# Kernel optimization log

Measured on AMD Instinct MI355X. Metric: run time of the kernel, lower is better.

The kernel has to match this reference:

```python
import jax, jax.numpy as jnp
import numpy as np

EMBED_DIM = 1024
NUM_HEADS = 16
HEAD_DIM = EMBED_DIM // NUM_HEADS
B, S = 4, 2048


def setup_inputs() -> dict:
    key = jax.random.key(0)
    ks = jax.random.split(key, 11)
    scale = 1.0 / np.sqrt(EMBED_DIM)
    def lin(k):
        kw, kb = jax.random.split(k)
        W = jax.random.uniform(kw, (EMBED_DIM, EMBED_DIM), jnp.float32, -scale, scale)
        b = jax.random.uniform(kb, (EMBED_DIM,), jnp.float32, -scale, scale)
        return W, b
    Wq, bq = lin(ks[0]); Wk, bk = lin(ks[1]); Wv, bv = lin(ks[2]); Wo, bo = lin(ks[3])
    return {
        "query": jax.random.normal(ks[4], (B, S, EMBED_DIM), jnp.float32),
        "key": jax.random.normal(ks[5], (B, S, EMBED_DIM), jnp.float32),
        "value": jax.random.normal(ks[6], (B, S, EMBED_DIM), jnp.float32),
        "Wq": Wq, "bq": bq, "Wk": Wk, "bk": bk, "Wv": Wv, "bv": bv, "Wo": Wo, "bo": bo,
    }


def reference(query, key, value, Wq, bq, Wk, bk, Wv, bv, Wo, bo):
    Bz, Sz, E = query.shape
    H, Dh = NUM_HEADS, HEAD_DIM
    # projections -> [B, H, S, Dh]
    q = (query @ Wq + bq).reshape(Bz, Sz, H, Dh).transpose(0, 2, 1, 3)
    k = (key @ Wk + bk).reshape(Bz, Sz, H, Dh).transpose(0, 2, 1, 3)
    v = (value @ Wv + bv).reshape(Bz, Sz, H, Dh).transpose(0, 2, 1, 3)
    scores = jnp.einsum('bhsd,bhtd->bhst', q, k) / jnp.sqrt(jnp.asarray(Dh, q.dtype))
    attn = jax.nn.softmax(scores, axis=-1)  # dropout is identity in eval mode
    out = jnp.einsum('bhst,bhtd->bhsd', attn, v)  # [B,H,S,Dh]
    out = out.transpose(0, 2, 1, 3).reshape(Bz, Sz, E)
    out = out @ Wo + bo
    return out, attn
```

## Files before the change

kernel.cpp:

```cpp
#include <hip/hip_runtime.h>
#include <stdint.h>


using bf16x8 = __attribute__((ext_vector_type(8))) short;
using f32x4  = __attribute__((ext_vector_type(4))) float;
using u16x4  = __attribute__((ext_vector_type(4))) unsigned short;
using u64x2  = __attribute__((ext_vector_type(2))) unsigned long long;

#define MFMA_BF16 __builtin_amdgcn_mfma_f32_16x16x32_bf16

__device__ __forceinline__ unsigned short f2bf(float x) {
    unsigned int u = __builtin_bit_cast(unsigned int, x);
    u = (u + 0x7FFFu + ((u >> 16) & 1u)) >> 16;
    return (unsigned short)u;
}
__device__ __forceinline__ float bf2f(unsigned short u) {
    return __builtin_bit_cast(float, (unsigned int)u << 16);
}
__device__ __forceinline__ float exp2_fast(float x) {
    float r; asm("v_exp_f32 %0, %1" : "=v"(r) : "v"(x)); return r;
}
__device__ __forceinline__ float log2_fast(float x) {
    float r; asm("v_log_f32 %0, %1" : "=v"(r) : "v"(x)); return r;
}
__device__ __forceinline__ void gload_lds16(const unsigned short* g, bf16x8* l) {
    __builtin_amdgcn_global_load_lds(
        (const __attribute__((address_space(1))) unsigned int*)(g),
        (__attribute__((address_space(3))) unsigned int*)(l), 16, 0, 0);
}

__global__ __launch_bounds__(256) void cvt_kernel(
    const float* __restrict__ q, const float* __restrict__ k,
    const float* __restrict__ v, unsigned short* __restrict__ dst)
{
    const float* src = (blockIdx.y == 0) ? q : (blockIdx.y == 1) ? k : v;
    unsigned short* d = dst + (size_t)blockIdx.y * 8388608;
    size_t i = ((size_t)blockIdx.x * 256 + threadIdx.x) * 8;
    float4 a = *(const float4*)(src + i);
    float4 b = *(const float4*)(src + i + 4);
    u16x4 lo = {f2bf(a.x), f2bf(a.y), f2bf(a.z), f2bf(a.w)};
    u16x4 hi = {f2bf(b.x), f2bf(b.y), f2bf(b.z), f2bf(b.w)};
    *(u16x4*)(d + i) = lo;
    *(u16x4*)(d + i + 4) = hi;
}

__global__ __launch_bounds__(256) void wtrans_kernel(
    const float* __restrict__ w0, const float* __restrict__ w1,
    const float* __restrict__ w2, const float* __restrict__ w3,
    unsigned short* __restrict__ Wt)
{
    __shared__ float tile[64][65];
    const float* src = (blockIdx.z == 0) ? w0 : (blockIdx.z == 1) ? w1 :
                       (blockIdx.z == 2) ? w2 : w3;
    unsigned short* dst = Wt + (size_t)blockIdx.z * (1u << 20);
    const int k0 = blockIdx.x * 64, n0 = blockIdx.y * 64;
    const int tid = threadIdx.x;
#pragma unroll
    for (int i = 0; i < 16; ++i) {
        int idx = i * 256 + tid;
        int kk = idx >> 6, nn = idx & 63;
        tile[kk][nn] = src[(size_t)(k0 + kk) * 1024 + n0 + nn];
    }
    __syncthreads();
#pragma unroll
    for (int i = 0; i < 16; ++i) {
        int idx = i * 256 + tid;
        int nn = idx >> 6, kk = idx & 63;
        dst[(size_t)(n0 + nn) * 1024 + k0 + kk] = f2bf(tile[kk][nn]);
    }
}

template<int OUT_MODE>
__global__ __launch_bounds__(256) void gemm_kernel(
    const unsigned short* __restrict__ A, const unsigned short* __restrict__ Bt,
    const float* __restrict__ bias, void* __restrict__ Cp, float prescale)
{
    __shared__ bf16x8 Alds[1024];
    __shared__ bf16x8 Blds[1024];
    const int tid = threadIdx.x;
    const int lane = tid & 63;
    const int w = tid >> 6;
    const int wm = w >> 1, wn = w & 1;
    const int m0 = blockIdx.x * 128, n0 = blockIdx.y * 128;
    const int r16 = lane & 15, g = lane >> 4;

    f32x4 acc[4][4] = {};

    for (int kt = 0; kt < 16; ++kt) {
        const int k0 = kt * 64;
#pragma unroll
        for (int issue = 0; issue < 4; ++issue) {
            int s = issue * 256 + tid;
            int row = s >> 3, cc = (s & 7) ^ (row & 7);
            gload_lds16(A  + (size_t)(m0 + row) * 1024 + k0 + cc * 8,
                        &Alds[issue * 256 + w * 64]);
            gload_lds16(Bt + (size_t)(n0 + row) * 1024 + k0 + cc * 8,
                        &Blds[issue * 256 + w * 64]);
        }
        __syncthreads();
#pragma unroll
        for (int ks = 0; ks < 2; ++ks) {
            bf16x8 af[4], bfr[4];
#pragma unroll
            for (int mf = 0; mf < 4; ++mf) {
                int row = wm * 64 + mf * 16 + r16;
                af[mf] = Alds[row * 8 + ((ks * 4 + g) ^ (row & 7))];
            }
#pragma unroll
            for (int nf = 0; nf < 4; ++nf) {
                int row = wn * 64 + nf * 16 + r16;
                bfr[nf] = Blds[row * 8 + ((ks * 4 + g) ^ (row & 7))];
            }
#pragma unroll
            for (int mf = 0; mf < 4; ++mf)
#pragma unroll
                for (int nf = 0; nf < 4; ++nf)
                    acc[mf][nf] = MFMA_BF16(af[mf], bfr[nf], acc[mf][nf], 0, 0, 0);
        }
        __syncthreads();
    }

#pragma unroll
    for (int nf = 0; nf < 4; ++nf) {
        const int n = n0 + wn * 64 + nf * 16 + r16;
        const float bv = bias[n];
#pragma unroll
        for (int mf = 0; mf < 4; ++mf) {
            const int mb = m0 + wm * 64 + mf * 16 + g * 4;
            if constexpr (OUT_MODE == 2) {
                float* C = (float*)Cp;
#pragma unroll
                for (int r = 0; r < 4; ++r)
                    C[(size_t)(mb + r) * 1024 + n] = acc[mf][nf][r] + bv;
            } else if constexpr (OUT_MODE == 0) {
                unsigned short* C = (unsigned short*)Cp;
                const int h = n >> 6, d = n & 63;
#pragma unroll
                for (int r = 0; r < 4; ++r) {
                    int m = mb + r;
                    int b = m >> 11, s2 = m & 2047;
                    C[((((size_t)b * 16 + h) * 2048 + s2) << 6) + d] =
                        f2bf((acc[mf][nf][r] + bv) * prescale);
                }
            } else {
                unsigned short* C = (unsigned short*)Cp;
                const int h = n >> 6, d = n & 63;
                const int b = mb >> 11, s2 = mb & 2047;
                u16x4 pk;
#pragma unroll
                for (int r = 0; r < 4; ++r) pk[r] = f2bf(acc[mf][nf][r] + bv);
                *(u16x4*)(C + (((size_t)b * 16 + h) * 64 + d) * 2048 + s2) = pk;
            }
        }
    }
}

__global__ __launch_bounds__(256) void attn_kernel(
    const unsigned short* __restrict__ Q,
    const unsigned short* __restrict__ K,
    const unsigned short* __restrict__ VT,
    float* __restrict__ attn,
    unsigned short* __restrict__ ctx)
{
    __shared__ bf16x8 k_buf[2][64 * 8];
    __shared__ bf16x8 v_buf[2][64 * 8];
    __shared__ unsigned long long p_buf[64 * 16];

    const int tid = threadIdx.x;
    const int lane = tid & 63;
    const int w = tid >> 6;
    const int L = blockIdx.x;
    const int xcd = L & 7, j = L >> 3;
    const int qt = j & 31;
    const int bh = ((j >> 5) << 3) | xcd;
    const int r16 = lane & 15, g = lane >> 4;

    const unsigned short* Kb = K + (size_t)bh * 2048 * 64;
    const unsigned short* Vb = VT + (size_t)bh * 64 * 2048;

    const int row0 = tid >> 3, cc0 = tid & 7;
    const int row1 = row0 + 32;
    const int kslot0 = row0 * 8 + (cc0 ^ (row0 & 7));
    const int kslot1 = row1 * 8 + (cc0 ^ (row1 & 7));

    const int qrow = w * 16 + r16;
    const unsigned short* qptr = Q + ((size_t)bh * 2048 + (size_t)qt * 64 + qrow) * 64 + g * 8;
    const bf16x8 qf0 = *(const bf16x8*)(qptr);
    const bf16x8 qf1 = *(const bf16x8*)(qptr + 32);

    k_buf[0][kslot0] = *(const bf16x8*)(Kb + (size_t)row0 * 64 + cc0 * 8);
    k_buf[0][kslot1] = *(const bf16x8*)(Kb + (size_t)row1 * 64 + cc0 * 8);
    bf16x8 pf0 = *(const bf16x8*)(Kb + 4096 + (size_t)row0 * 64 + cc0 * 8);
    bf16x8 pf1 = *(const bf16x8*)(Kb + 4096 + (size_t)row1 * 64 + cc0 * 8);
    __syncthreads();

    float l4[4] = {0.f, 0.f, 0.f, 0.f};
#pragma unroll 2
    for (int kt = 0; kt < 32; ++kt) {
        const int cur = kt & 1;
        bf16x8 nn0, nn1;
        if (kt + 2 < 32) {
            const unsigned short* src = Kb + (size_t)(kt + 2) * 4096;
            nn0 = *(const bf16x8*)(src + (size_t)row0 * 64 + cc0 * 8);
            nn1 = *(const bf16x8*)(src + (size_t)row1 * 64 + cc0 * 8);
        }
#pragma unroll
        for (int kf = 0; kf < 4; ++kf) {
            const int row = kf * 16 + r16;
            f32x4 t = {};
            t = MFMA_BF16(k_buf[cur][row * 8 + ((0 + g) ^ (row & 7))], qf0, t, 0, 0, 0);
            t = MFMA_BF16(k_buf[cur][row * 8 + ((4 + g) ^ (row & 7))], qf1, t, 0, 0, 0);
#pragma unroll
            for (int r = 0; r < 4; ++r) l4[r] += exp2_fast(t[r]);
        }
        if (kt + 1 < 32) {
            k_buf[cur ^ 1][kslot0] = pf0;
            k_buf[cur ^ 1][kslot1] = pf1;
        }
        __syncthreads();
        pf0 = nn0;
        pf1 = nn1;
    }
    float l_acc = (l4[0] + l4[1]) + (l4[2] + l4[3]);
    l_acc += __shfl_xor(l_acc, 16, 64);
    l_acc += __shfl_xor(l_acc, 32, 64);
    const float lg2invl = -log2_fast(l_acc);

    {
        bf16x8 a0 = *(const bf16x8*)(Kb + (size_t)row0 * 64 + cc0 * 8);
        bf16x8 a1 = *(const bf16x8*)(Kb + (size_t)row1 * 64 + cc0 * 8);
        bf16x8 b0 = *(const bf16x8*)(Vb + (size_t)row0 * 2048 + cc0 * 8);
        bf16x8 b1 = *(const bf16x8*)(Vb + (size_t)row1 * 2048 + cc0 * 8);
        k_buf[0][kslot0] = a0; k_buf[0][kslot1] = a1;
        v_buf[0][kslot0] = b0; v_buf[0][kslot1] = b1;
    }
    __syncthreads();

    float* attn_tile = attn + ((size_t)bh * 2048 + (size_t)qt * 64) * 2048;
    const f32x4 cinit = {lg2invl, lg2invl, lg2invl, lg2invl};

    f32x4 oacc[4] = {};
    for (int kt = 0; kt < 32; ++kt) {
        const int cur = kt & 1;
        bf16x8 nk0, nk1, nv0, nv1;
        if (kt != 31) {
            const unsigned short* ksrc = Kb + (size_t)(kt + 1) * 64 * 64;
            const unsigned short* vsrc = Vb + (size_t)(kt + 1) * 64;
            nk0 = *(const bf16x8*)(ksrc + (size_t)row0 * 64 + cc0 * 8);
            nk1 = *(const bf16x8*)(ksrc + (size_t)row1 * 64 + cc0 * 8);
            nv0 = *(const bf16x8*)(vsrc + (size_t)row0 * 2048 + cc0 * 8);
            nv1 = *(const bf16x8*)(vsrc + (size_t)row1 * 2048 + cc0 * 8);
        }
#pragma unroll
        for (int kf = 0; kf < 4; ++kf) {
            const int row = kf * 16 + r16;
            f32x4 t = cinit;
            t = MFMA_BF16(k_buf[cur][row * 8 + ((0 + g) ^ (row & 7))], qf0, t, 0, 0, 0);
            t = MFMA_BF16(k_buf[cur][row * 8 + ((4 + g) ^ (row & 7))], qf1, t, 0, 0, 0);
            u16x4 pk;
#pragma unroll
            for (int r = 0; r < 4; ++r) pk[r] = f2bf(exp2_fast(t[r]));
            const int c = 2 * kf + (g >> 1);
            p_buf[qrow * 16 + ((c ^ (qrow & 7)) << 1) + (g & 1)] =
                __builtin_bit_cast(unsigned long long, pk);
        }
#pragma unroll
        for (int i = 0; i < 2; ++i)
#pragma unroll
            for (int jj = 0; jj < 2; ++jj) {
                const int srow = w * 16 + i * 8 + (lane >> 3);
                const int col0 = jj * 32 + (lane & 7) * 4;
                const int c = col0 >> 3, half = (col0 >> 2) & 1;
                unsigned long long praw =
                    p_buf[srow * 16 + ((c ^ (srow & 7)) << 1) + half];
                u16x4 pk = __builtin_bit_cast(u16x4, praw);
                f32x4 pv = {bf2f(pk[0]), bf2f(pk[1]), bf2f(pk[2]), bf2f(pk[3])};
                __builtin_nontemporal_store(
                    pv, (f32x4*)(attn_tile + (size_t)srow * 2048 + kt * 64 + col0));
            }
#pragma unroll
        for (int ks = 0; ks < 2; ++ks) {
            const int cs = (ks * 4 + g) ^ (qrow & 7);
            u64x2 praw2 = {p_buf[qrow * 16 + cs * 2], p_buf[qrow * 16 + cs * 2 + 1]};
            bf16x8 a = __builtin_bit_cast(bf16x8, praw2);
#pragma unroll
            for (int df = 0; df < 4; ++df) {
                const int rowv = df * 16 + r16;
                oacc[df] = MFMA_BF16(a, v_buf[cur][rowv * 8 + ((ks * 4 + g) ^ (rowv & 7))],
                                     oacc[df], 0, 0, 0);
            }
        }
        if (kt != 31) {
            k_buf[cur ^ 1][kslot0] = nk0; k_buf[cur ^ 1][kslot1] = nk1;
            v_buf[cur ^ 1][kslot0] = nv0; v_buf[cur ^ 1][kslot1] = nv1;
        }
        __syncthreads();
    }

    const int b = bh >> 4, h = bh & 15;
#pragma unroll
    for (int df = 0; df < 4; ++df) {
        int d = df * 16 + r16;
#pragma unroll
        for (int r = 0; r < 4; ++r) {
            int s2 = qt * 64 + w * 16 + g * 4 + r;
            ctx[((size_t)b * 2048 + s2) * 1024 + h * 64 + d] = f2bf(oacc[df][r]);
        }
    }
}

extern "C" void kernel_launch(void* const* d_in, const int* in_sizes, int n_in,
                              void* d_out, int out_size, void* d_ws, size_t ws_size,
                              hipStream_t stream)
{
    (void)in_sizes; (void)n_in; (void)out_size; (void)ws_size;
    const float* query = (const float*)d_in[0];
    const float* key_  = (const float*)d_in[1];
    const float* value = (const float*)d_in[2];
    const float* Wq = (const float*)d_in[3];
    const float* bq = (const float*)d_in[4];
    const float* Wk = (const float*)d_in[5];
    const float* bk = (const float*)d_in[6];
    const float* Wv = (const float*)d_in[7];
    const float* bv = (const float*)d_in[8];
    const float* Wo = (const float*)d_in[9];
    const float* bo = (const float*)d_in[10];

    char* ws = (char*)d_ws;
    unsigned short* Wt  = (unsigned short*)(ws);
    unsigned short* qb  = (unsigned short*)(ws + ((size_t)8  << 20));
    unsigned short* kb  = (unsigned short*)(ws + ((size_t)24 << 20));
    unsigned short* vtb = (unsigned short*)(ws + ((size_t)40 << 20));
    unsigned short* ctx = (unsigned short*)(ws + ((size_t)56 << 20));
    float* outp = (float*)d_out;
    float* attn = outp + (size_t)4 * 2048 * 1024;

    const size_t ATTN_ELEMS = (size_t)64 * 2048 * 2048;
    const size_t STASH_FLOATS = (size_t)3 * 8388608 / 2;
    unsigned short* qkvb = (unsigned short*)(attn + (ATTN_ELEMS - STASH_FLOATS));
    unsigned short* qbf = qkvb;
    unsigned short* kbf = qkvb + 8388608;
    unsigned short* vbf = qkvb + 16777216;

    const float qscale = 0.125f * 1.44269504089f;

    cvt_kernel<<<dim3(4096, 3), 256, 0, stream>>>(query, key_, value, qkvb);
    wtrans_kernel<<<dim3(16, 16, 4), 256, 0, stream>>>(Wq, Wk, Wv, Wo, Wt);
    gemm_kernel<0><<<dim3(64, 8), 256, 0, stream>>>(qbf, Wt,              bq, qb,  qscale);
    gemm_kernel<0><<<dim3(64, 8), 256, 0, stream>>>(kbf, Wt + (1u << 20), bk, kb,  1.0f);
    gemm_kernel<1><<<dim3(64, 8), 256, 0, stream>>>(vbf, Wt + (2u << 20), bv, vtb, 1.0f);
    attn_kernel<<<dim3(2048), 256, 0, stream>>>(qb, kb, vtb, attn, ctx);
    gemm_kernel<2><<<dim3(64, 8), 256, 0, stream>>>(ctx, Wt + (3u << 20), bo, outp, 1.0f);
}
```

Before: 369.0 us.

## Split attention softmax row-sum pass into separate kernel

The softmax denominator pass moves out of the attention kernel into its own pass1 kernel. That kernel writes per-row sums to a small workspace buffer, which reuses the region of already-consumed transposed Wq weights. The main attention kernel then reads the sums and does only the probability write and P·V pass. This may lower register and shared-memory pressure in each kernel and improve occupancy, at the cost of an extra launch and reloading Q and K.

```diff
diff --git a/kernel.cpp b/kernel.cpp
--- a/kernel.cpp
+++ b/kernel.cpp
@@ -155,16 +155,12 @@
     }
 }
 
-__global__ __launch_bounds__(256) void attn_kernel(
+__global__ __launch_bounds__(256) void pass1_kernel(
     const unsigned short* __restrict__ Q,
     const unsigned short* __restrict__ K,
-    const unsigned short* __restrict__ VT,
-    float* __restrict__ attn,
-    unsigned short* __restrict__ ctx)
+    float* __restrict__ lbuf)
 {
     __shared__ bf16x8 k_buf[2][64 * 8];
-    __shared__ bf16x8 v_buf[2][64 * 8];
-    __shared__ unsigned long long p_buf[64 * 16];
 
     const int tid = threadIdx.x;
     const int lane = tid & 63;
@@ -176,7 +172,6 @@
     const int r16 = lane & 15, g = lane >> 4;
 
     const unsigned short* Kb = K + (size_t)bh * 2048 * 64;
-    const unsigned short* Vb = VT + (size_t)bh * 64 * 2048;
 
     const int row0 = tid >> 3, cc0 = tid & 7;
     const int row1 = row0 + 32;
@@ -224,7 +219,45 @@
     float l_acc = (l4[0] + l4[1]) + (l4[2] + l4[3]);
     l_acc += __shfl_xor(l_acc, 16, 64);
     l_acc += __shfl_xor(l_acc, 32, 64);
-    const float lg2invl = -log2_fast(l_acc);
+    if (lane < 16)
+        lbuf[(size_t)bh * 2048 + qt * 64 + w * 16 + lane] = l_acc;
+}
+
+__global__ __launch_bounds__(256) void attn_kernel(
+    const unsigned short* __restrict__ Q,
+    const unsigned short* __restrict__ K,
+    const unsigned short* __restrict__ VT,
+    const float* __restrict__ lbuf,
+    float* __restrict__ attn,
+    unsigned short* __restrict__ ctx)
+{
+    __shared__ bf16x8 k_buf[2][64 * 8];
+    __shared__ bf16x8 v_buf[2][64 * 8];
+    __shared__ unsigned long long p_buf[64 * 16];
+
+    const int tid = threadIdx.x;
+    const int lane = tid & 63;
+    const int w = tid >> 6;
+    const int L = blockIdx.x;
+    const int xcd = L & 7, j = L >> 3;
+    const int qt = j & 31;
+    const int bh = ((j >> 5) << 3) | xcd;
+    const int r16 = lane & 15, g = lane >> 4;
+
+    const unsigned short* Kb = K + (size_t)bh * 2048 * 64;
+    const unsigned short* Vb = VT + (size_t)bh * 64 * 2048;
+
+    const int row0 = tid >> 3, cc0 = tid & 7;
+    const int row1 = row0 + 32;
+    const int kslot0 = row0 * 8 + (cc0 ^ (row0 & 7));
+    const int kslot1 = row1 * 8 + (cc0 ^ (row1 & 7));
+
+    const int qrow = w * 16 + r16;
+    const unsigned short* qptr = Q + ((size_t)bh * 2048 + (size_t)qt * 64 + qrow) * 64 + g * 8;
+    const bf16x8 qf0 = *(const bf16x8*)(qptr);
+    const bf16x8 qf1 = *(const bf16x8*)(qptr + 32);
+
+    const float lg2invl = -log2_fast(lbuf[(size_t)bh * 2048 + qt * 64 + qrow]);
 
     {
         bf16x8 a0 = *(const bf16x8*)(Kb + (size_t)row0 * 64 + cc0 * 8);
@@ -332,6 +365,7 @@
     unsigned short* kb  = (unsigned short*)(ws + ((size_t)24 << 20));
     unsigned short* vtb = (unsigned short*)(ws + ((size_t)40 << 20));
     unsigned short* ctx = (unsigned short*)(ws + ((size_t)56 << 20));
+    float* lbuf = (float*)ws;
     float* outp = (float*)d_out;
     float* attn = outp + (size_t)4 * 2048 * 1024;
 
@@ -349,6 +383,7 @@
     gemm_kernel<0><<<dim3(64, 8), 256, 0, stream>>>(qbf, Wt,              bq, qb,  qscale);
     gemm_kernel<0><<<dim3(64, 8), 256, 0, stream>>>(kbf, Wt + (1u << 20), bk, kb,  1.0f);
     gemm_kernel<1><<<dim3(64, 8), 256, 0, stream>>>(vbf, Wt + (2u << 20), bv, vtb, 1.0f);
-    attn_kernel<<<dim3(2048), 256, 0, stream>>>(qb, kb, vtb, attn, ctx);
+    pass1_kernel<<<dim3(2048), 256, 0, stream>>>(qb, kb, lbuf);
+    attn_kernel<<<dim3(2048), 256, 0, stream>>>(qb, kb, vtb, lbuf, attn, ctx);
     gemm_kernel<2><<<dim3(64, 8), 256, 0, stream>>>(ctx, Wt + (3u << 20), bo, outp, 1.0f);
 }
```

After: 419.6 us. 1.14x slower.
